# Optimization experiments

Measured on AMD Instinct MI355X. Metric: run time of the kernel, lower is better.

Reference implementation:

```python
import jax, jax.numpy as jnp
import numpy as np

N_QUBITS = 16
REPS = 2
BATCH = 512


def _apply_1q_batched(state, gates, q):
    """Apply per-sample 2x2 gates [B,2,2] to qubit q of state [B]+[2]*n."""
    state = jnp.moveaxis(state, 1 + q, -1)
    state = jnp.einsum('bij,b...j->b...i', gates, state)
    return jnp.moveaxis(state, -1, 1 + q)


def _apply_1q(state, gate, q):
    """Apply a shared 2x2 gate to qubit q of state [B]+[2]*n."""
    state = jnp.moveaxis(state, 1 + q, -1)
    state = jnp.einsum('ij,b...j->b...i', gate, state)
    return jnp.moveaxis(state, -1, 1 + q)


def _apply_cnot(state, c, t):
    """CNOT with control c, target t on state [B]+[2]*n."""
    state = jnp.moveaxis(state, (1 + c, 1 + t), (-2, -1))
    state = jnp.stack([state[..., 0, :], state[..., 1, ::-1]], axis=-2)
    return jnp.moveaxis(state, (-2, -1), (1 + c, 1 + t))


def _rx_gates(theta):
    """RX(theta) gates; theta [...,] -> gates [...,2,2] complex64."""
    c = jnp.cos(theta / 2).astype(jnp.complex64)
    s = (-1j * jnp.sin(theta / 2)).astype(jnp.complex64)
    row0 = jnp.stack([c, s], axis=-1)
    row1 = jnp.stack([s, c], axis=-1)
    return jnp.stack([row0, row1], axis=-2)


def _pauliz_signs(n):
    idx = np.arange(2 ** n)
    # pennylane convention: wire 0 is the most significant bit
    bits = (idx[None, :] >> (n - 1 - np.arange(n)[:, None])) & 1  # [n, 2^n]
    return jnp.asarray(1.0 - 2.0 * bits, dtype=jnp.float32)


def setup_inputs() -> dict:
    key = jax.random.key(0)
    kz, kp, kw = jax.random.split(key, 3)
    z = jax.random.normal(kz, (BATCH, N_QUBITS), dtype=jnp.float32)
    params = jax.random.normal(kp, (N_QUBITS,), dtype=jnp.float32) * 0.1
    ent_weights = jax.random.normal(kw, (REPS, N_QUBITS), dtype=jnp.float32) * 0.1
    return {"z": z, "params": params, "ent_weights": ent_weights}


def reference(z, params, ent_weights):
    B, n = z.shape
    # |0...0> initial state, batched
    state = jnp.zeros((B, 2 ** n), dtype=jnp.complex64).at[:, 0].set(1.0)
    state = state.reshape([B] + [2] * n)

    # Embedding layer: RX(z[b,i] + params[i]) on each wire (per-sample angles)
    angles = z + params[None, :]  # [B, n]
    for q in range(n):
        state = _apply_1q_batched(state, _rx_gates(angles[:, q]), q)

    # BasicEntanglerLayers, reps=2: per layer, RX(w) on each wire then ring CNOTs
    for l in range(REPS):
        for q in range(n):
            state = _apply_1q(state, _rx_gates(ent_weights[l, q]), q)
        for q in range(n):
            state = _apply_cnot(state, q, (q + 1) % n)

    # <Z_i> for each wire
    probs = jnp.abs(state.reshape(B, -1)) ** 2  # [B, 2^n] float32
    signs = _pauliz_signs(n)  # [n, 2^n]
    return probs @ signs.T  # [B, n]
```

## Files before the change

kernel.cpp:

```cpp
#include <hip/hip_runtime.h>

#define NQ 16

__device__ __forceinline__ float2 rxmix(float2 v0, float2 v1, float c, float s) {
    return make_float2(c * v0.x + s * v1.y, c * v0.y - s * v1.x);
}

extern "C" __global__ __launch_bounds__(256)
void qsim_kernel(const float* __restrict__ z,
                 const float* __restrict__ params,
                 const float* __restrict__ ew,
                 float* __restrict__ out)
{
    const int b    = blockIdx.x;
    const int tid  = threadIdx.x;
    const int lane = tid & 63;
    const int wv   = tid >> 6;

    __shared__ float c1[NQ], s1[NQ], cw[NQ], sw[NQ];
    __shared__ __align__(16) float2 V4[4][258];
    __shared__ __align__(16) float  PART[4][7][33];
    __shared__ float2 G[2][9][10];

    if (tid < 32) {
        const int q = tid & 15;
        if (tid < 16) {
            float phi = 0.5f * (z[b * NQ + q] + params[q] + ew[q]);
            float ss, cc;
            sincosf(phi, &ss, &cc);
            c1[q] = cc; s1[q] = ss;
        } else {
            float w = 0.5f * ew[NQ + q];
            float ss, cc;
            sincosf(w, &ss, &cc);
            cw[q] = cc; sw[q] = ss;
        }
    }
    __syncthreads();

    const bool hiw = (wv < 2);
    const int  par = wv & 1;
    const int  wb  = hiw ? 0 : 8;

    const int b5 = (lane >> 5) & 1;
    const int gl = (lane ^ (lane >> 1)) & 31;
    float t0 = ((gl >> 4) & 1) ? s1[wb + 3] : c1[wb + 3];
    float t1 = ((gl >> 3) & 1) ? s1[wb + 4] : c1[wb + 4];
    float t2 = ((gl >> 2) & 1) ? s1[wb + 5] : c1[wb + 5];
    float t3 = ((gl >> 1) & 1) ? s1[wb + 6] : c1[wb + 6];
    float t4 = ( gl       & 1) ? s1[wb + 7] : c1[wb + 7];
    const float laneMag = (t0 * t1) * (t2 * t3) * t4;
    const int   laneKK  = __popc(gl);

    const int p1 = hiw ? par : 0;
    float w0v0 = par ? s1[wb]     : c1[wb];
    float w0v1 = par ? c1[wb]     : s1[wb];
    float w1v0 = p1  ? s1[wb + 1] : c1[wb + 1];
    float w1v1 = p1  ? c1[wb + 1] : s1[wb + 1];
    float m2v0 = b5  ? s1[wb + 2] : c1[wb + 2];
    float m2v1 = b5  ? c1[wb + 2] : s1[wb + 2];

    float2 v[4];
#pragma unroll
    for (int k = 0; k < 4; ++k) {
        const int a = k >> 1, bb = k & 1, ab = a ^ bb;
        float wa = a  ? w0v1 : w0v0;
        float wc = ab ? w1v1 : w1v0;
        float wd = bb ? m2v1 : m2v0;
        float mag = laneMag * ((wa * wc) * wd);
        int kk = laneKK + (a ^ par) + (ab ^ p1) + (bb ^ b5);
        float sg = (kk & 2) ? -mag : mag;
        v[k] = (kk & 1) ? make_float2(0.f, -sg) : make_float2(sg, 0.f);
    }

    {
        float c = cw[wb + 0], s = sw[wb + 0];
        float2 n0 = rxmix(v[0], v[2], c, s), n2 = rxmix(v[2], v[0], c, s);
        float2 n1 = rxmix(v[1], v[3], c, s), n3 = rxmix(v[3], v[1], c, s);
        v[0] = n0; v[1] = n1; v[2] = n2; v[3] = n3;
    }
    {
        float c = cw[wb + 1], s = sw[wb + 1];
        float2 n0 = rxmix(v[0], v[1], c, s), n1 = rxmix(v[1], v[0], c, s);
        float2 n2 = rxmix(v[2], v[3], c, s), n3 = rxmix(v[3], v[2], c, s);
        v[0] = n0; v[1] = n1; v[2] = n2; v[3] = n3;
    }
#pragma unroll
    for (int bbit = 5; bbit >= 1; --bbit) {
        float c = cw[wb + 7 - bbit], s = sw[wb + 7 - bbit];
        int m = 1 << bbit;
#pragma unroll
        for (int k = 0; k < 4; ++k) {
            float px = __shfl_xor(v[k].x, m);
            float py = __shfl_xor(v[k].y, m);
            v[k] = make_float2(c * v[k].x + s * py, c * v[k].y - s * px);
        }
    }
#pragma unroll
    for (int k = 0; k < 4; ++k) V4[wv][(k << 6) | lane] = v[k];
    __syncthreads();

    const int e0 = tid & 1, j2 = tid & ~1;
    float4 rA0 = *(const float4*)&V4[0][j2];
    float4 rA1 = *(const float4*)&V4[1][j2];
    float4 rB0 = *(const float4*)&V4[2][j2];
    float4 rB1 = *(const float4*)&V4[3][j2];
    float c7 = cw[7], s7 = sw[7], c15 = cw[15], s15 = sw[15];

    float2 x[4], yv[4];
    {
        float2 a0 = make_float2(rA0.x, rA0.y), b0 = make_float2(rA0.z, rA0.w);
        float2 a1 = make_float2(rA1.x, rA1.y), b1 = make_float2(rA1.z, rA1.w);
        if (e0 == 0) {
            x[0] = make_float2(c7 * a0.x, c7 * a0.y);
            x[1] = make_float2(c7 * a1.x, c7 * a1.y);
            x[2] = make_float2(s7 * b0.y, -s7 * b0.x);
            x[3] = make_float2(s7 * b1.y, -s7 * b1.x);
        } else {
            x[0] = make_float2(s7 * a0.y, -s7 * a0.x);
            x[1] = make_float2(s7 * a1.y, -s7 * a1.x);
            x[2] = make_float2(c7 * b0.x, c7 * b0.y);
            x[3] = make_float2(c7 * b1.x, c7 * b1.y);
        }
        float2 g0 = make_float2(rB0.x, rB0.y), d0 = make_float2(rB0.z, rB0.w);
        float2 g1 = make_float2(rB1.x, rB1.y), d1 = make_float2(rB1.z, rB1.w);
        if (e0 == 0) {
            yv[0] = make_float2(c15 * g0.x, c15 * g0.y);
            yv[2] = make_float2(c15 * g1.x, c15 * g1.y);
            yv[1] = make_float2(s15 * d0.y, -s15 * d0.x);
            yv[3] = make_float2(s15 * d1.y, -s15 * d1.x);
        } else {
            yv[0] = make_float2(s15 * g0.y, -s15 * g0.x);
            yv[2] = make_float2(s15 * g1.y, -s15 * g1.x);
            yv[1] = make_float2(c15 * d0.x, c15 * d0.y);
            yv[3] = make_float2(c15 * d1.x, c15 * d1.y);
        }
    }

    float wr[32];
    {
        float2 *p = x;
#pragma unroll
        for (int side = 0; side < 2; ++side, p = yv) {
            int o = side * 16;
            wr[o + 0] = p[0].x * p[0].x + p[0].y * p[0].y;
            wr[o + 1] = p[1].x * p[1].x + p[1].y * p[1].y;
            wr[o + 2] = p[2].x * p[2].x + p[2].y * p[2].y;
            wr[o + 3] = p[3].x * p[3].x + p[3].y * p[3].y;
            wr[o + 4]  = p[0].x * p[1].x + p[0].y * p[1].y;
            wr[o + 5]  = p[0].y * p[1].x - p[0].x * p[1].y;
            wr[o + 6]  = p[0].x * p[2].x + p[0].y * p[2].y;
            wr[o + 7]  = p[0].y * p[2].x - p[0].x * p[2].y;
            wr[o + 8]  = p[0].x * p[3].x + p[0].y * p[3].y;
            wr[o + 9]  = p[0].y * p[3].x - p[0].x * p[3].y;
            wr[o + 10] = p[1].x * p[2].x + p[1].y * p[2].y;
            wr[o + 11] = p[1].y * p[2].x - p[1].x * p[2].y;
            wr[o + 12] = p[1].x * p[3].x + p[1].y * p[3].y;
            wr[o + 13] = p[1].y * p[3].x - p[1].x * p[3].y;
            wr[o + 14] = p[2].x * p[3].x + p[2].y * p[3].y;
            wr[o + 15] = p[2].y * p[3].x - p[2].x * p[3].y;
        }
    }

#pragma unroll
    for (int lev = 0; lev < 6; ++lev) {
        int m = 1 << lev;
        float s = (lane & m) ? -1.f : 1.f;
#pragma unroll
        for (int a = 0; a < 32; ++a) {
            float wp = __shfl_xor(wr[a], m);
            wr[a] = fmaf(s, wr[a], wp);
        }
    }
    {
        const int p = __popc(lane);
        if (lane == ((63 >> (6 - p)) << (6 - p))) {
#pragma unroll
            for (int a = 0; a < 32; ++a) PART[wv][p][a] = wr[a];
        }
    }
    __syncthreads();

    if (tid < 180) {
        int side = tid / 90, rest = tid - side * 90;
        int pp = rest / 9, m = rest - pp * 9;
        int M;
        if (side == 0) M = (m < 8) ? (((1 << (m + 1)) - 1) << (7 - m)) : 0x7F;
        else           M = (m == 0) ? 0 : (((1 << m) - 1) << (8 - m));
        int low = M & 63, hi2 = M >> 6;
        int li2 = __popc(low);
        int rs   = (int)((0x3E2CA18640ULL >> (4 * pp)) & 0xF);
        bool diag = (0x291 >> pp) & 1;
        float gr = 0.f, gi = 0.f;
#pragma unroll
        for (int w2 = 0; w2 < 4; ++w2) {
            float s = (__popc(hi2 & w2) & 1) ? -1.f : 1.f;
            gr = fmaf(s, PART[w2][li2][side * 16 + rs], gr);
            if (!diag) gi = fmaf(s, PART[w2][li2][side * 16 + rs + 1], gi);
        }
        G[side][m][pp] = make_float2(gr, gi);
    }
    __syncthreads();

    if (tid < NQ) {
        const int i = tid;
        int hm, lm;
        if (i == 0)      { hm = 8; lm = 8; }
        else if (i <= 7) { hm = i; lm = 0; }
        else             { hm = 7; lm = i - 7; }
        float r = 0.f;
#pragma unroll
        for (int pp = 0; pp < 10; ++pp) {
            float2 gh = G[0][hm][pp];
            float2 gl = G[1][lm][pp];
            float re = gh.x * gl.x - gh.y * gl.y;
            float wgt = ((0x291 >> pp) & 1) ? 1.f : 2.f;
            r = fmaf(wgt, re, r);
        }
        out[b * NQ + i] = r;
    }
}

extern "C" void kernel_launch(void* const* d_in, const int* in_sizes, int n_in,
                              void* d_out, int out_size, void* d_ws, size_t ws_size,
                              hipStream_t stream) {
    const float* z      = (const float*)d_in[0];
    const float* params = (const float*)d_in[1];
    const float* ew     = (const float*)d_in[2];
    float* out          = (float*)d_out;
    const int B = in_sizes[0] / NQ;
    qsim_kernel<<<B, 256, 0, stream>>>(z, params, ew, out);
}
```

Measured before the change: 63.27 us.

## Double threads per block, halving per-thread state and reduction work

Each block now uses 512 threads instead of 256. Every wave holds 2 amplitudes instead of 4, and the wire-7 split moves into the lane/wave index. Each thread computes its own sincos and broadcasts the angles by wave shuffles, which removes the initial shared-memory stage and one barrier. The second stage splits the two sides across thread halves, so each thread reduces 16 values instead of 32. The cost is more threads per sample and redundant sincos in every wave, against shorter per-thread critical paths and fewer registers.

Measured after the change: 64.90 us. 1.03x slower.

```diff
diff --git a/kernel.cpp b/kernel.cpp
--- a/kernel.cpp
+++ b/kernel.cpp
@@ -6,7 +6,7 @@
     return make_float2(c * v0.x + s * v1.y, c * v0.y - s * v1.x);
 }
 
-extern "C" __global__ __launch_bounds__(256)
+extern "C" __global__ __launch_bounds__(512, 4)
 void qsim_kernel(const float* __restrict__ z,
                  const float* __restrict__ params,
                  const float* __restrict__ ew,
@@ -17,157 +17,163 @@
     const int lane = tid & 63;
     const int wv   = tid >> 6;
 
-    __shared__ float c1[NQ], s1[NQ], cw[NQ], sw[NQ];
-    __shared__ __align__(16) float2 V4[4][258];
-    __shared__ __align__(16) float  PART[4][7][33];
+    __shared__ float2 V4[4][2][128];
+    __shared__ float  PART[4][7][2][17];
     __shared__ float2 G[2][9][10];
 
-    if (tid < 32) {
-        const int q = tid & 15;
-        if (tid < 16) {
-            float phi = 0.5f * (z[b * NQ + q] + params[q] + ew[q]);
-            float ss, cc;
-            sincosf(phi, &ss, &cc);
-            c1[q] = cc; s1[q] = ss;
+    const int  arr = wv >> 1;
+    const int  e0w = wv & 1;
+    const bool hiw = (arr < 2);
+    const int  par = arr & 1;
+    const int  p1  = hiw ? par : 0;
+    const int  wb  = hiw ? 0 : 8;
+
+    float myA = 0.f;
+    if (lane < 8) {
+        const int q = wb + lane;
+        myA = 0.5f * (z[b * NQ + q] + params[q] + ew[q]);
+    } else if (lane < 16) {
+        const int q = wb + (lane - 8);
+        myA = 0.5f * ew[NQ + q];
+    }
+    float myS, myC;
+    sincosf(myA, &myS, &myC);
+
+    const float c1_0 = __shfl(myC, 0), s1_0 = __shfl(myS, 0);
+    const float c1_1 = __shfl(myC, 1), s1_1 = __shfl(myS, 1);
+    const float c1_2 = __shfl(myC, 2), s1_2 = __shfl(myS, 2);
+    const float c1_3 = __shfl(myC, 3), s1_3 = __shfl(myS, 3);
+    const float c1_4 = __shfl(myC, 4), s1_4 = __shfl(myS, 4);
+    const float c1_5 = __shfl(myC, 5), s1_5 = __shfl(myS, 5);
+    const float c1_6 = __shfl(myC, 6), s1_6 = __shfl(myS, 6);
+    const float c1_7 = __shfl(myC, 7), s1_7 = __shfl(myS, 7);
+    const float cw0  = __shfl(myC, 8),  sw0 = __shfl(myS, 8);
+    const float cw1  = __shfl(myC, 9),  sw1 = __shfl(myS, 9);
+    const float cw2  = __shfl(myC, 10), sw2 = __shfl(myS, 10);
+    const float cw3  = __shfl(myC, 11), sw3 = __shfl(myS, 11);
+    const float cw4  = __shfl(myC, 12), sw4 = __shfl(myS, 12);
+    const float cw5  = __shfl(myC, 13), sw5 = __shfl(myS, 13);
+    const float cw6  = __shfl(myC, 14), sw6 = __shfl(myS, 14);
+
+    const int gl  = (lane ^ (lane >> 1)) & 31;
+    const int l5  = (lane >> 5) & 1;
+    const int eb7 = (lane & 1) ^ e0w;
+
+    float t0 = ((gl >> 4) & 1) ? s1_2 : c1_2;
+    float t1 = ((gl >> 3) & 1) ? s1_3 : c1_3;
+    float t2 = ((gl >> 2) & 1) ? s1_4 : c1_4;
+    float t3 = ((gl >> 1) & 1) ? s1_5 : c1_5;
+    float t4 = ((gl >> 0) & 1) ? s1_6 : c1_6;
+    float t5 = eb7 ? s1_7 : c1_7;
+    const float laneMag = ((t0 * t1) * (t2 * t3)) * (t4 * t5);
+    const int   laneKK  = __popc(gl) + eb7;
+
+    const float f00 = par ? s1_0 : c1_0;
+    const float f01 = par ? c1_0 : s1_0;
+    const int   e1k0 = l5 ^ p1;
+    const float f10 = e1k0 ? s1_1 : c1_1;
+    const float f11 = e1k0 ? c1_1 : s1_1;
+
+    float mag0 = laneMag * (f00 * f10);
+    float mag1 = laneMag * (f01 * f11);
+    int kk0 = laneKK + par + e1k0;
+    int kk1 = laneKK + (1 ^ par) + (1 ^ e1k0);
+    float sg0 = (kk0 & 2) ? -mag0 : mag0;
+    float sg1 = (kk1 & 2) ? -mag1 : mag1;
+    float2 v0r = (kk0 & 1) ? make_float2(0.f, -sg0) : make_float2(sg0, 0.f);
+    float2 v1r = (kk1 & 1) ? make_float2(0.f, -sg1) : make_float2(sg1, 0.f);
+
+    {
+        float2 n0 = rxmix(v0r, v1r, cw0, sw0);
+        float2 n1 = rxmix(v1r, v0r, cw0, sw0);
+        v0r = n0; v1r = n1;
+    }
+#define ROT(cc, ss, mm) do {                                              \
+        float px = __shfl_xor(v0r.x, mm), py = __shfl_xor(v0r.y, mm);     \
+        v0r = make_float2((cc) * v0r.x + (ss) * py,                       \
+                          (cc) * v0r.y - (ss) * px);                      \
+        px = __shfl_xor(v1r.x, mm); py = __shfl_xor(v1r.y, mm);           \
+        v1r = make_float2((cc) * v1r.x + (ss) * py,                       \
+                          (cc) * v1r.y - (ss) * px);                      \
+    } while (0)
+    ROT(cw1, sw1, 32);
+    ROT(cw2, sw2, 16);
+    ROT(cw3, sw3, 8);
+    ROT(cw4, sw4, 4);
+    ROT(cw5, sw5, 2);
+    ROT(cw6, sw6, 1);
+#undef ROT
+
+    V4[arr][e0w][lane]      = v0r;
+    V4[arr][e0w][64 + lane] = v1r;
+    __syncthreads();
+
+    const int e  = tid & 255;
+    const int ph = tid >> 8;
+    const int f  = e >> 1;
+    const int e0 = e & 1;
+    const int w2 = wv & 3;
+
+    const float cS = __shfl(myC, 15);
+    const float sS = __shfl(myS, 15);
+
+    const int baseArr = ph ? 2 : 0;
+    const float2 r0a = V4[baseArr][0][f];
+    const float2 r0b = V4[baseArr][1][f];
+    const float2 r1a = V4[baseArr + 1][0][f];
+    const float2 r1b = V4[baseArr + 1][1][f];
+
+    float2 p0, p1v, p2, p3;
+    if (ph == 0) {
+        if (e0 == 0) {
+            p0  = make_float2(cS * r0a.x, cS * r0a.y);
+            p1v = make_float2(cS * r1a.x, cS * r1a.y);
+            p2  = make_float2(sS * r0b.y, -sS * r0b.x);
+            p3  = make_float2(sS * r1b.y, -sS * r1b.x);
         } else {
-            float w = 0.5f * ew[NQ + q];
-            float ss, cc;
-            sincosf(w, &ss, &cc);
-            cw[q] = cc; sw[q] = ss;
-        }
-    }
-    __syncthreads();
-
-    const bool hiw = (wv < 2);
-    const int  par = wv & 1;
-    const int  wb  = hiw ? 0 : 8;
-
-    const int b5 = (lane >> 5) & 1;
-    const int gl = (lane ^ (lane >> 1)) & 31;
-    float t0 = ((gl >> 4) & 1) ? s1[wb + 3] : c1[wb + 3];
-    float t1 = ((gl >> 3) & 1) ? s1[wb + 4] : c1[wb + 4];
-    float t2 = ((gl >> 2) & 1) ? s1[wb + 5] : c1[wb + 5];
-    float t3 = ((gl >> 1) & 1) ? s1[wb + 6] : c1[wb + 6];
-    float t4 = ( gl       & 1) ? s1[wb + 7] : c1[wb + 7];
-    const float laneMag = (t0 * t1) * (t2 * t3) * t4;
-    const int   laneKK  = __popc(gl);
-
-    const int p1 = hiw ? par : 0;
-    float w0v0 = par ? s1[wb]     : c1[wb];
-    float w0v1 = par ? c1[wb]     : s1[wb];
-    float w1v0 = p1  ? s1[wb + 1] : c1[wb + 1];
-    float w1v1 = p1  ? c1[wb + 1] : s1[wb + 1];
-    float m2v0 = b5  ? s1[wb + 2] : c1[wb + 2];
-    float m2v1 = b5  ? c1[wb + 2] : s1[wb + 2];
-
-    float2 v[4];
-#pragma unroll
-    for (int k = 0; k < 4; ++k) {
-        const int a = k >> 1, bb = k & 1, ab = a ^ bb;
-        float wa = a  ? w0v1 : w0v0;
-        float wc = ab ? w1v1 : w1v0;
-        float wd = bb ? m2v1 : m2v0;
-        float mag = laneMag * ((wa * wc) * wd);
-        int kk = laneKK + (a ^ par) + (ab ^ p1) + (bb ^ b5);
-        float sg = (kk & 2) ? -mag : mag;
-        v[k] = (kk & 1) ? make_float2(0.f, -sg) : make_float2(sg, 0.f);
-    }
-
-    {
-        float c = cw[wb + 0], s = sw[wb + 0];
-        float2 n0 = rxmix(v[0], v[2], c, s), n2 = rxmix(v[2], v[0], c, s);
-        float2 n1 = rxmix(v[1], v[3], c, s), n3 = rxmix(v[3], v[1], c, s);
-        v[0] = n0; v[1] = n1; v[2] = n2; v[3] = n3;
-    }
-    {
-        float c = cw[wb + 1], s = sw[wb + 1];
-        float2 n0 = rxmix(v[0], v[1], c, s), n1 = rxmix(v[1], v[0], c, s);
-        float2 n2 = rxmix(v[2], v[3], c, s), n3 = rxmix(v[3], v[2], c, s);
-        v[0] = n0; v[1] = n1; v[2] = n2; v[3] = n3;
-    }
-#pragma unroll
-    for (int bbit = 5; bbit >= 1; --bbit) {
-        float c = cw[wb + 7 - bbit], s = sw[wb + 7 - bbit];
-        int m = 1 << bbit;
-#pragma unroll
-        for (int k = 0; k < 4; ++k) {
-            float px = __shfl_xor(v[k].x, m);
-            float py = __shfl_xor(v[k].y, m);
-            v[k] = make_float2(c * v[k].x + s * py, c * v[k].y - s * px);
-        }
-    }
-#pragma unroll
-    for (int k = 0; k < 4; ++k) V4[wv][(k << 6) | lane] = v[k];
-    __syncthreads();
-
-    const int e0 = tid & 1, j2 = tid & ~1;
-    float4 rA0 = *(const float4*)&V4[0][j2];
-    float4 rA1 = *(const float4*)&V4[1][j2];
-    float4 rB0 = *(const float4*)&V4[2][j2];
-    float4 rB1 = *(const float4*)&V4[3][j2];
-    float c7 = cw[7], s7 = sw[7], c15 = cw[15], s15 = sw[15];
-
-    float2 x[4], yv[4];
-    {
-        float2 a0 = make_float2(rA0.x, rA0.y), b0 = make_float2(rA0.z, rA0.w);
-        float2 a1 = make_float2(rA1.x, rA1.y), b1 = make_float2(rA1.z, rA1.w);
+            p0  = make_float2(sS * r0a.y, -sS * r0a.x);
+            p1v = make_float2(sS * r1a.y, -sS * r1a.x);
+            p2  = make_float2(cS * r0b.x, cS * r0b.y);
+            p3  = make_float2(cS * r1b.x, cS * r1b.y);
+        }
+    } else {
         if (e0 == 0) {
-            x[0] = make_float2(c7 * a0.x, c7 * a0.y);
-            x[1] = make_float2(c7 * a1.x, c7 * a1.y);
-            x[2] = make_float2(s7 * b0.y, -s7 * b0.x);
-            x[3] = make_float2(s7 * b1.y, -s7 * b1.x);
+            p0  = make_float2(cS * r0a.x, cS * r0a.y);
+            p2  = make_float2(cS * r1a.x, cS * r1a.y);
+            p1v = make_float2(sS * r0b.y, -sS * r0b.x);
+            p3  = make_float2(sS * r1b.y, -sS * r1b.x);
         } else {
-            x[0] = make_float2(s7 * a0.y, -s7 * a0.x);
-            x[1] = make_float2(s7 * a1.y, -s7 * a1.x);
-            x[2] = make_float2(c7 * b0.x, c7 * b0.y);
-            x[3] = make_float2(c7 * b1.x, c7 * b1.y);
-        }
-        float2 g0 = make_float2(rB0.x, rB0.y), d0 = make_float2(rB0.z, rB0.w);
-        float2 g1 = make_float2(rB1.x, rB1.y), d1 = make_float2(rB1.z, rB1.w);
-        if (e0 == 0) {
-            yv[0] = make_float2(c15 * g0.x, c15 * g0.y);
-            yv[2] = make_float2(c15 * g1.x, c15 * g1.y);
-            yv[1] = make_float2(s15 * d0.y, -s15 * d0.x);
-            yv[3] = make_float2(s15 * d1.y, -s15 * d1.x);
-        } else {
-            yv[0] = make_float2(s15 * g0.y, -s15 * g0.x);
-            yv[2] = make_float2(s15 * g1.y, -s15 * g1.x);
-            yv[1] = make_float2(c15 * d0.x, c15 * d0.y);
-            yv[3] = make_float2(c15 * d1.x, c15 * d1.y);
-        }
-    }
-
-    float wr[32];
-    {
-        float2 *p = x;
-#pragma unroll
-        for (int side = 0; side < 2; ++side, p = yv) {
-            int o = side * 16;
-            wr[o + 0] = p[0].x * p[0].x + p[0].y * p[0].y;
-            wr[o + 1] = p[1].x * p[1].x + p[1].y * p[1].y;
-            wr[o + 2] = p[2].x * p[2].x + p[2].y * p[2].y;
-            wr[o + 3] = p[3].x * p[3].x + p[3].y * p[3].y;
-            wr[o + 4]  = p[0].x * p[1].x + p[0].y * p[1].y;
-            wr[o + 5]  = p[0].y * p[1].x - p[0].x * p[1].y;
-            wr[o + 6]  = p[0].x * p[2].x + p[0].y * p[2].y;
-            wr[o + 7]  = p[0].y * p[2].x - p[0].x * p[2].y;
-            wr[o + 8]  = p[0].x * p[3].x + p[0].y * p[3].y;
-            wr[o + 9]  = p[0].y * p[3].x - p[0].x * p[3].y;
-            wr[o + 10] = p[1].x * p[2].x + p[1].y * p[2].y;
-            wr[o + 11] = p[1].y * p[2].x - p[1].x * p[2].y;
-            wr[o + 12] = p[1].x * p[3].x + p[1].y * p[3].y;
-            wr[o + 13] = p[1].y * p[3].x - p[1].x * p[3].y;
-            wr[o + 14] = p[2].x * p[3].x + p[2].y * p[3].y;
-            wr[o + 15] = p[2].y * p[3].x - p[2].x * p[3].y;
-        }
-    }
+            p0  = make_float2(sS * r0a.y, -sS * r0a.x);
+            p2  = make_float2(sS * r1a.y, -sS * r1a.x);
+            p1v = make_float2(cS * r0b.x, cS * r0b.y);
+            p3  = make_float2(cS * r1b.x, cS * r1b.y);
+        }
+    }
+
+    float wr[16];
+    wr[0]  = p0.x * p0.x + p0.y * p0.y;
+    wr[1]  = p1v.x * p1v.x + p1v.y * p1v.y;
+    wr[2]  = p2.x * p2.x + p2.y * p2.y;
+    wr[3]  = p3.x * p3.x + p3.y * p3.y;
+    wr[4]  = p0.x * p1v.x + p0.y * p1v.y;
+    wr[5]  = p0.y * p1v.x - p0.x * p1v.y;
+    wr[6]  = p0.x * p2.x + p0.y * p2.y;
+    wr[7]  = p0.y * p2.x - p0.x * p2.y;
+    wr[8]  = p0.x * p3.x + p0.y * p3.y;
+    wr[9]  = p0.y * p3.x - p0.x * p3.y;
+    wr[10] = p1v.x * p2.x + p1v.y * p2.y;
+    wr[11] = p1v.y * p2.x - p1v.x * p2.y;
+    wr[12] = p1v.x * p3.x + p1v.y * p3.y;
+    wr[13] = p1v.y * p3.x - p1v.x * p3.y;
+    wr[14] = p2.x * p3.x + p2.y * p3.y;
+    wr[15] = p2.y * p3.x - p2.x * p3.y;
 
 #pragma unroll
     for (int lev = 0; lev < 6; ++lev) {
         int m = 1 << lev;
         float s = (lane & m) ? -1.f : 1.f;
 #pragma unroll
-        for (int a = 0; a < 32; ++a) {
+        for (int a = 0; a < 16; ++a) {
             float wp = __shfl_xor(wr[a], m);
             wr[a] = fmaf(s, wr[a], wp);
         }
@@ -176,7 +182,7 @@
         const int p = __popc(lane);
         if (lane == ((63 >> (6 - p)) << (6 - p))) {
 #pragma unroll
-            for (int a = 0; a < 32; ++a) PART[wv][p][a] = wr[a];
+            for (int a = 0; a < 16; ++a) PART[w2][p][ph][a] = wr[a];
         }
     }
     __syncthreads();
@@ -193,10 +199,10 @@
         bool diag = (0x291 >> pp) & 1;
         float gr = 0.f, gi = 0.f;
 #pragma unroll
-        for (int w2 = 0; w2 < 4; ++w2) {
-            float s = (__popc(hi2 & w2) & 1) ? -1.f : 1.f;
-            gr = fmaf(s, PART[w2][li2][side * 16 + rs], gr);
-            if (!diag) gi = fmaf(s, PART[w2][li2][side * 16 + rs + 1], gi);
+        for (int w = 0; w < 4; ++w) {
+            float s = (__popc(hi2 & w) & 1) ? -1.f : 1.f;
+            gr = fmaf(s, PART[w][li2][side][rs], gr);
+            if (!diag) gi = fmaf(s, PART[w][li2][side][rs + 1], gi);
         }
         G[side][m][pp] = make_float2(gr, gi);
     }
@@ -229,5 +235,5 @@
     const float* ew     = (const float*)d_in[2];
     float* out          = (float*)d_out;
     const int B = in_sizes[0] / NQ;
-    qsim_kernel<<<B, 256, 0, stream>>>(z, params, ew, out);
+    qsim_kernel<<<B, 512, 0, stream>>>(z, params, ew, out);
 }
```
